# Optimization experiments

Hardware: AMD Instinct MI355X
Metric: run time of the kernel (lower is better)

## Reference

```python
import jax, jax.numpy as jnp
import numpy as np

N = 50000   # nodes
E = 800000  # edges
F = 128     # num_features
H = 128     # n_hidden_channels
C = 16      # num_classes


def _gcn_conv(x, W, b, src, dst, dinv):
    """PyG GCNConv: h = x @ W; out = D^-1/2 (A+I) D^-1/2 h + b."""
    h = x @ W                                   # [N, out]
    coef = dinv[src] * dinv[dst]                # [E]
    msg = h[src] * coef[:, None]                # gather + scale
    agg = jax.ops.segment_sum(msg, dst, num_segments=N)
    agg = agg + h * (dinv * dinv)[:, None]      # self-loop term
    return agg + b


def setup_inputs() -> dict:
    key = jax.random.key(0)
    ks = jax.random.split(key, 8)
    x = jax.random.normal(ks[0], (N, F), dtype=jnp.float32)
    edge_index = jax.random.randint(ks[1], (2, E), 0, N, dtype=jnp.int64)

    def glorot(k, fan_in, fan_out):
        return jax.random.normal(k, (fan_in, fan_out), dtype=jnp.float32) / np.sqrt(fan_in)

    return {
        "x": x,
        "edge_index": edge_index,
        "W1": glorot(ks[2], F, H), "b1": jnp.zeros((H,), jnp.float32),
        "W2": glorot(ks[3], H, H), "b2": jnp.zeros((H,), jnp.float32),
        "W3": glorot(ks[4], H, H), "b3": jnp.zeros((H,), jnp.float32),
        "W4": glorot(ks[5], H, C), "b4": jnp.zeros((C,), jnp.float32),
        "Wc": glorot(ks[6], C, 1), "bc": jnp.zeros((1,), jnp.float32),
    }


def reference(x, edge_index, W1, b1, W2, b2, W3, b3, W4, b4, Wc, bc):
    src, dst = edge_index[0], edge_index[1]
    # degree with self-loops (edge_weight = 1)
    deg = jax.ops.segment_sum(jnp.ones((E,), x.dtype), dst, num_segments=N) + 1.0
    dinv = jax.lax.rsqrt(deg)

    out = _gcn_conv(x, W1, b1, src, dst, dinv)
    out = jnp.tanh(_gcn_conv(out, W2, b2, src, dst, dinv))
    out = jax.nn.leaky_relu(_gcn_conv(out, W3, b3, src, dst, dinv), negative_slope=0.01)
    out = jax.nn.leaky_relu(_gcn_conv(out, W4, b4, src, dst, dinv), negative_slope=0.01)
    out = jax.nn.elu(out @ Wc + bc)             # [N, 1]
    return out
```

## Files before the change

### kernel.cpp

```cpp
#include <hip/hip_runtime.h>
#include <hip/hip_bf16.h>
#include <cstdint>
#include <cstddef>

#define NN 50000
#define NE 800000

using short8v = __attribute__((ext_vector_type(8))) short;
using f32x4 = __attribute__((ext_vector_type(4))) float;

__device__ __forceinline__ unsigned short f2bf(float f) {
    unsigned u = __float_as_uint(f);
    u += 0x7fffu + ((u >> 16) & 1u);
    return (unsigned short)(u >> 16);
}
__device__ __forceinline__ float bf2f(unsigned s) {
    return __uint_as_float(s << 16);
}


__global__ __launch_bounds__(256) void zero_i32(int* __restrict__ p, int n) {
    int i = blockIdx.x * 256 + threadIdx.x;
    if (i < n) p[i] = 0;
}

__global__ __launch_bounds__(256) void count_deg_rank(const int* __restrict__ dst,
                                                      int* __restrict__ cntP,
                                                      int* __restrict__ rank, int E) {
    int e = blockIdx.x * 256 + threadIdx.x;
    if (e < E) {
        int d = dst[e];
        rank[e] = atomicAdd(&cntP[d << 4], 1);
    }
}

__global__ __launch_bounds__(1024) void scan1(const int* __restrict__ cntP,
                                              int* __restrict__ local,
                                              int* __restrict__ bsum,
                                              float* __restrict__ dinv, int N) {
    int t = threadIdx.x;
    int g = blockIdx.x * 1024 + t;
    int lane = t & 63, w = t >> 6;
    int v = (g < N) ? cntP[g << 4] : 0;
    if (g < N) dinv[g] = rsqrtf((float)v + 1.0f);
    int x = v;
    #pragma unroll
    for (int off = 1; off < 64; off <<= 1) {
        int y = __shfl_up(x, off);
        if (lane >= off) x += y;
    }
    __shared__ int wsum[16];
    if (lane == 63) wsum[w] = x;
    __syncthreads();
    if (t < 16) {
        int s = wsum[t];
        int xx = s;
        #pragma unroll
        for (int off = 1; off < 16; off <<= 1) {
            int y = __shfl_up(xx, off);
            if (t >= off) xx += y;
        }
        wsum[t] = xx - s;
    }
    __syncthreads();
    int excl = wsum[w] + x - v;
    if (g < N) local[g] = excl;
    if (t == 1023) bsum[blockIdx.x] = excl + v;
}

__global__ __launch_bounds__(64) void scan2(int* __restrict__ bsum, int NB) {
    int t = threadIdx.x;
    int v = (t < NB) ? bsum[t] : 0;
    int x = v;
    #pragma unroll
    for (int off = 1; off < 64; off <<= 1) {
        int y = __shfl_up(x, off);
        if (t >= off) x += y;
    }
    if (t < NB) bsum[t] = x - v;
}

__global__ __launch_bounds__(256) void scan3(const int* __restrict__ local,
                                             const int* __restrict__ bsum,
                                             int* __restrict__ rowptr, int N, int E) {
    int g = blockIdx.x * 256 + threadIdx.x;
    if (g < N) rowptr[g] = local[g] + bsum[g >> 10];
    if (g == 0) rowptr[N] = E;
}

__global__ __launch_bounds__(256) void scatter_plain(const int* __restrict__ src,
                                                     const int* __restrict__ dst,
                                                     const int* __restrict__ rowptr,
                                                     const int* __restrict__ rank,
                                                     int* __restrict__ csr, int E) {
    int e = blockIdx.x * 256 + threadIdx.x;
    if (e < E) {
        int d = dst[e];
        csr[rowptr[d] + rank[e]] = src[e];
    }
}


__global__ __launch_bounds__(256) void split_wt(const float* __restrict__ Wa,
                                                const float* __restrict__ Wb,
                                                const float* __restrict__ Wc,
                                                unsigned short* __restrict__ WTh,
                                                unsigned short* __restrict__ WTl) {
    const float* W = (blockIdx.y == 0) ? Wa : (blockIdx.y == 1) ? Wb : Wc;
    int i = blockIdx.x * 256 + threadIdx.x;
    int n = i >> 7, k = i & 127;
    float v = W[k * 128 + n];
    unsigned short h = f2bf(v);
    float lo = v - bf2f(h);
    size_t base = (size_t)blockIdx.y * 16384 + i;
    WTh[base] = h;
    WTl[base] = f2bf(lo);
}


template <bool F32IN>
__global__ __launch_bounds__(256) void gemm_mfma(const void* __restrict__ Xin,
                                                 const void* __restrict__ Xlin,
                                                 const unsigned short* __restrict__ WTh,
                                                 const unsigned short* __restrict__ WTl,
                                                 const float* __restrict__ dinv,
                                                 float* __restrict__ out, int N) {
    __shared__ unsigned short xh[64 * 128];
    __shared__ unsigned short xl[64 * 128];
    int tid = threadIdx.x;
    int lane = tid & 63, wv = tid >> 6;
    int row0 = blockIdx.x * 64;

    #pragma unroll
    for (int i = 0; i < 4; ++i) {
        int id = i * 256 + tid;
        int r = id >> 4, kc = id & 15;
        uint4 vh = make_uint4(0, 0, 0, 0), vl = make_uint4(0, 0, 0, 0);
        if (row0 + r < N) {
            if constexpr (F32IN) {
                const float* Xf = (const float*)Xin;
                float4 a = *(const float4*)(Xf + (size_t)(row0 + r) * 128 + kc * 8);
                float4 b = *(const float4*)(Xf + (size_t)(row0 + r) * 128 + kc * 8 + 4);
                unsigned short h0 = f2bf(a.x), h1 = f2bf(a.y), h2 = f2bf(a.z), h3 = f2bf(a.w);
                unsigned short h4 = f2bf(b.x), h5 = f2bf(b.y), h6 = f2bf(b.z), h7 = f2bf(b.w);
                vh = make_uint4((unsigned)h0 | ((unsigned)h1 << 16),
                                (unsigned)h2 | ((unsigned)h3 << 16),
                                (unsigned)h4 | ((unsigned)h5 << 16),
                                (unsigned)h6 | ((unsigned)h7 << 16));
                vl = make_uint4((unsigned)f2bf(a.x - bf2f(h0)) | ((unsigned)f2bf(a.y - bf2f(h1)) << 16),
                                (unsigned)f2bf(a.z - bf2f(h2)) | ((unsigned)f2bf(a.w - bf2f(h3)) << 16),
                                (unsigned)f2bf(b.x - bf2f(h4)) | ((unsigned)f2bf(b.y - bf2f(h5)) << 16),
                                (unsigned)f2bf(b.z - bf2f(h6)) | ((unsigned)f2bf(b.w - bf2f(h7)) << 16));
            } else {
                vh = *(const uint4*)&((const unsigned*)Xin)[(size_t)(row0 + r) * 64 + kc * 4];
                vl = *(const uint4*)&((const unsigned*)Xlin)[(size_t)(row0 + r) * 64 + kc * 4];
            }
        }
        int off = r * 128 + ((kc * 8) ^ ((r & 7) << 3));
        *(uint4*)&xh[off] = vh;
        *(uint4*)&xl[off] = vl;
    }
    __syncthreads();

    int mstrip = (wv & 1) * 32;
    int nbase = (wv >> 1) * 64;
    f32x4 acc[2][4] = {};

    #pragma unroll
    for (int ks = 0; ks < 4; ++ks) {
        short8v afh[2], afl[2];
        #pragma unroll
        for (int mt = 0; mt < 2; ++mt) {
            int r = mstrip + mt * 16 + (lane & 15);
            int off = r * 128 + ((ks * 32 + ((lane >> 4) * 8)) ^ ((r & 7) << 3));
            afh[mt] = *(const short8v*)&xh[off];
            afl[mt] = *(const short8v*)&xl[off];
        }
        #pragma unroll
        for (int nt = 0; nt < 4; ++nt) {
            int c = nbase + nt * 16 + (lane & 15);
            size_t goff = (size_t)c * 128 + ks * 32 + (lane >> 4) * 8;
            short8v bfh = *(const short8v*)&WTh[goff];
            short8v bfl = *(const short8v*)&WTl[goff];
            #pragma unroll
            for (int mt = 0; mt < 2; ++mt) {
                acc[mt][nt] = __builtin_amdgcn_mfma_f32_16x16x32_bf16(afh[mt], bfh, acc[mt][nt], 0, 0, 0);
                acc[mt][nt] = __builtin_amdgcn_mfma_f32_16x16x32_bf16(afh[mt], bfl, acc[mt][nt], 0, 0, 0);
                acc[mt][nt] = __builtin_amdgcn_mfma_f32_16x16x32_bf16(afl[mt], bfh, acc[mt][nt], 0, 0, 0);
            }
        }
    }

    #pragma unroll
    for (int mt = 0; mt < 2; ++mt) {
        #pragma unroll
        for (int i = 0; i < 4; ++i) {
            int r = row0 + mstrip + mt * 16 + (lane >> 4) * 4 + i;
            if (r < N) {
                float dv = dinv[r];
                #pragma unroll
                for (int nt = 0; nt < 4; ++nt) {
                    int cg = nbase + nt * 16 + (lane & 15);
                    out[(size_t)r * 128 + cg] = acc[mt][nt][i] * dv;
                }
            }
        }
    }
}

__global__ __launch_bounds__(256) void gemm16(const unsigned* __restrict__ Xh,
                                              const unsigned* __restrict__ Xl,
                                              const float* __restrict__ W,
                                              const float* __restrict__ dinv,
                                              float* __restrict__ out, int N) {
    __shared__ float xs[64][128];
    __shared__ float ws4[128][16];
    int tid = threadIdx.x;
    int row0 = blockIdx.x * 64;

    #pragma unroll
    for (int i = 0; i < 2; ++i)
        ((float4*)ws4)[i * 256 + tid] = ((const float4*)W)[i * 256 + tid];

    #pragma unroll
    for (int i = 0; i < 8; ++i) {
        int id = i * 256 + tid;
        int r = id >> 5, c4 = id & 31;
        float4 v = make_float4(0.f, 0.f, 0.f, 0.f);
        if (row0 + r < N) {
            uint2 hh = *(const uint2*)&Xh[(size_t)(row0 + r) * 64 + c4 * 2];
            uint2 ll = *(const uint2*)&Xl[(size_t)(row0 + r) * 64 + c4 * 2];
            v.x = bf2f(hh.x & 0xffffu) + bf2f(ll.x & 0xffffu);
            v.y = bf2f(hh.x >> 16) + bf2f(ll.x >> 16);
            v.z = bf2f(hh.y & 0xffffu) + bf2f(ll.y & 0xffffu);
            v.w = bf2f(hh.y >> 16) + bf2f(ll.y >> 16);
        }
        *(float4*)&xs[r][c4 * 4] = v;
    }
    __syncthreads();

    int ty = tid >> 4, tx = tid & 15;
    float acc[4] = {};
    #pragma unroll 4
    for (int k = 0; k < 128; ++k) {
        float wvv = ws4[k][tx];
        #pragma unroll
        for (int i = 0; i < 4; ++i)
            acc[i] = fmaf(xs[ty * 4 + i][k], wvv, acc[i]);
    }
    #pragma unroll
    for (int i = 0; i < 4; ++i) {
        int r = row0 + ty * 4 + i;
        if (r < N) out[(size_t)r * 16 + tx] = acc[i] * dinv[r];
    }
}


template <int ACT>
__global__ __launch_bounds__(256) void agg128(const float* __restrict__ HS,
                                              const int* __restrict__ rp,
                                              const int* __restrict__ csr,
                                              const float* __restrict__ dinv,
                                              const float* __restrict__ b,
                                              unsigned* __restrict__ Xh,
                                              unsigned* __restrict__ Xl, int N) {
    int wid = threadIdx.x >> 6, lane = threadIdx.x & 63;
    int n = blockIdx.x * 4 + wid;
    if (n >= N) return;
    const float2* H2 = (const float2*)HS;
    float2 a0 = H2[(size_t)n * 64 + lane];
    float2 a1 = make_float2(0.f, 0.f), a2 = a1, a3 = a1;
    float2 a4 = a1, a5 = a1, a6 = a1, a7 = a1;
    int e = rp[n], end = rp[n + 1];
    for (; e + 8 <= end; e += 8) {
        int s0 = csr[e], s1 = csr[e + 1], s2 = csr[e + 2], s3 = csr[e + 3];
        int s4 = csr[e + 4], s5 = csr[e + 5], s6 = csr[e + 6], s7 = csr[e + 7];
        float2 v0 = H2[(size_t)s0 * 64 + lane];
        float2 v1 = H2[(size_t)s1 * 64 + lane];
        float2 v2 = H2[(size_t)s2 * 64 + lane];
        float2 v3 = H2[(size_t)s3 * 64 + lane];
        float2 v4 = H2[(size_t)s4 * 64 + lane];
        float2 v5 = H2[(size_t)s5 * 64 + lane];
        float2 v6 = H2[(size_t)s6 * 64 + lane];
        float2 v7 = H2[(size_t)s7 * 64 + lane];
        a0.x += v0.x; a0.y += v0.y; a1.x += v1.x; a1.y += v1.y;
        a2.x += v2.x; a2.y += v2.y; a3.x += v3.x; a3.y += v3.y;
        a4.x += v4.x; a4.y += v4.y; a5.x += v5.x; a5.y += v5.y;
        a6.x += v6.x; a6.y += v6.y; a7.x += v7.x; a7.y += v7.y;
    }
    if (e + 4 <= end) {
        int s0 = csr[e], s1 = csr[e + 1], s2 = csr[e + 2], s3 = csr[e + 3];
        float2 v0 = H2[(size_t)s0 * 64 + lane];
        float2 v1 = H2[(size_t)s1 * 64 + lane];
        float2 v2 = H2[(size_t)s2 * 64 + lane];
        float2 v3 = H2[(size_t)s3 * 64 + lane];
        a4.x += v0.x; a4.y += v0.y; a5.x += v1.x; a5.y += v1.y;
        a6.x += v2.x; a6.y += v2.y; a7.x += v3.x; a7.y += v3.y;
        e += 4;
    }
    for (; e < end; ++e) {
        int s = csr[e];
        float2 v = H2[(size_t)s * 64 + lane];
        a0.x += v.x; a0.y += v.y;
    }
    float accx = ((a0.x + a1.x) + (a2.x + a3.x)) + ((a4.x + a5.x) + (a6.x + a7.x));
    float accy = ((a0.y + a1.y) + (a2.y + a3.y)) + ((a4.y + a5.y) + (a6.y + a7.y));
    float dv = dinv[n];
    float2 bb = ((const float2*)b)[lane];
    float ox = fmaf(dv, accx, bb.x);
    float oy = fmaf(dv, accy, bb.y);
    if (ACT == 1) { ox = tanhf(ox); oy = tanhf(oy); }
    else if (ACT == 2) {
        ox = ox > 0.f ? ox : 0.01f * ox;
        oy = oy > 0.f ? oy : 0.01f * oy;
    }
    unsigned short h0 = f2bf(ox), h1 = f2bf(oy);
    float l0 = ox - bf2f(h0), l1 = oy - bf2f(h1);
    Xh[(size_t)n * 64 + lane] = (unsigned)h0 | ((unsigned)h1 << 16);
    Xl[(size_t)n * 64 + lane] = (unsigned)f2bf(l0) | ((unsigned)f2bf(l1) << 16);
}


__global__ __launch_bounds__(256) void final_layer(const float* __restrict__ HS4,
                                                   const int* __restrict__ rp,
                                                   const int* __restrict__ csr,
                                                   const float* __restrict__ dinv,
                                                   const float* __restrict__ b4,
                                                   const float* __restrict__ Wc,
                                                   const float* __restrict__ bc,
                                                   float* __restrict__ out, int N) {
    int wid = threadIdx.x >> 6, lane = threadIdx.x & 63;
    int n = blockIdx.x * 4 + wid;
    if (n >= N) return;
    int f = lane & 15, g = lane >> 4;
    float acc = 0.f;
    int beg = rp[n], end = rp[n + 1];
    for (int e = beg + g; e < end; e += 4)
        acc += HS4[(size_t)csr[e] * 16 + f];
    acc += __shfl_xor(acc, 16);
    acc += __shfl_xor(acc, 32);
    acc += HS4[(size_t)n * 16 + f];
    float t = fmaf(dinv[n], acc, b4[f]);
    t = t > 0.f ? t : 0.01f * t;
    float p = t * Wc[f];
    p += __shfl_xor(p, 1);
    p += __shfl_xor(p, 2);
    p += __shfl_xor(p, 4);
    p += __shfl_xor(p, 8);
    if (lane == 0) {
        float z = p + bc[0];
        out[n] = z > 0.f ? z : expm1f(z);
    }
}


extern "C" void kernel_launch(void* const* d_in, const int* in_sizes, int n_in,
                              void* d_out, int out_size, void* d_ws, size_t ws_size,
                              hipStream_t stream) {
    const int N = NN, E = NE;
    const float* x  = (const float*)d_in[0];
    const int*   ei = (const int*)d_in[1];
    const float* W1 = (const float*)d_in[2];
    const float* b1 = (const float*)d_in[3];
    const float* W2 = (const float*)d_in[4];
    const float* b2 = (const float*)d_in[5];
    const float* W3 = (const float*)d_in[6];
    const float* b3 = (const float*)d_in[7];
    const float* W4 = (const float*)d_in[8];
    const float* b4 = (const float*)d_in[9];
    const float* Wc = (const float*)d_in[10];
    const float* bc = (const float*)d_in[11];
    float* out = (float*)d_out;
    const int* src = ei;
    const int* dst = ei + E;

    char* p = (char*)d_ws;
    auto carve = [&](size_t bytes) -> char* {
        char* q = p;
        p += (bytes + 255) & ~(size_t)255;
        return q;
    };
    int*            cntP   = (int*)carve((size_t)N * 16 * 4);
    int*            rank   = (int*)carve((size_t)E * 4);
    int*            rowptr = (int*)carve((size_t)(N + 1) * 4);
    float*          dinv   = (float*)carve((size_t)N * 4);
    int*            csr    = (int*)carve((size_t)E * 4);
    int*            locsc  = (int*)carve((size_t)N * 4);
    int*            bsum   = (int*)carve((size_t)64 * 4);
    unsigned short* WTh    = (unsigned short*)carve((size_t)3 * 16384 * 2);
    unsigned short* WTl    = (unsigned short*)carve((size_t)3 * 16384 * 2);
    unsigned*       Xh     = (unsigned*)carve((size_t)N * 64 * 4);
    unsigned*       Xl     = (unsigned*)carve((size_t)N * 64 * 4);
    float*          bufB   = (float*)carve((size_t)N * 128 * 4);

    const int NB = (N + 1023) / 1024;

    zero_i32<<<(N * 16 + 255) / 256, 256, 0, stream>>>(cntP, N * 16);
    count_deg_rank<<<(E + 255) / 256, 256, 0, stream>>>(dst, cntP, rank, E);
    scan1<<<NB, 1024, 0, stream>>>(cntP, locsc, bsum, dinv, N);
    scan2<<<1, 64, 0, stream>>>(bsum, NB);
    scan3<<<(N + 255) / 256, 256, 0, stream>>>(locsc, bsum, rowptr, N, E);
    scatter_plain<<<(E + 255) / 256, 256, 0, stream>>>(src, dst, rowptr, rank, csr, E);
    split_wt<<<dim3(64, 3), 256, 0, stream>>>(W1, W2, W3, WTh, WTl);

    int gblocks = (N + 63) / 64;
    int ablocks = (N + 3) / 4;

    gemm_mfma<true><<<gblocks, 256, 0, stream>>>(x, nullptr, WTh, WTl, dinv, bufB, N);
    agg128<0><<<ablocks, 256, 0, stream>>>(bufB, rowptr, csr, dinv, b1, Xh, Xl, N);
    gemm_mfma<false><<<gblocks, 256, 0, stream>>>(Xh, Xl, WTh + 16384, WTl + 16384, dinv, bufB, N);
    agg128<1><<<ablocks, 256, 0, stream>>>(bufB, rowptr, csr, dinv, b2, Xh, Xl, N);
    gemm_mfma<false><<<gblocks, 256, 0, stream>>>(Xh, Xl, WTh + 32768, WTl + 32768, dinv, bufB, N);
    agg128<2><<<ablocks, 256, 0, stream>>>(bufB, rowptr, csr, dinv, b3, Xh, Xl, N);
    gemm16<<<gblocks, 256, 0, stream>>>(Xh, Xl, W4, dinv, bufB, N);
    final_layer<<<ablocks, 256, 0, stream>>>(bufB, rowptr, csr, dinv, b4, Wc, bc, out, N);
}
```

Before: 348.7 us.

## Merge setup kernels and stage weight tiles through LDS in GEMM

Replaces the zero kernel with hipMemsetAsync, folds the single-block scan2 into each scan3 block, and merges the weight-split kernel into the CSR scatter kernel as extra blocks. Together these cut several kernel launches from the preprocessing chain. The MFMA GEMM now loads each 32-wide K slice of the transposed weights into padded shared memory, instead of reading B fragments directly from global memory. That adds two barriers per K step and extra LDS use, which may lower occupancy.

New measurement: 330.8 us. -5.1%, faster.

```diff
diff --git a/kernel.cpp b/kernel.cpp
--- a/kernel.cpp
+++ b/kernel.cpp
@@ -18,11 +18,6 @@
     return __uint_as_float(s << 16);
 }
 
-
-__global__ __launch_bounds__(256) void zero_i32(int* __restrict__ p, int n) {
-    int i = blockIdx.x * 256 + threadIdx.x;
-    if (i < n) p[i] = 0;
-}
 
 __global__ __launch_bounds__(256) void count_deg_rank(const int* __restrict__ dst,
                                                       int* __restrict__ cntP,
@@ -68,53 +63,56 @@
     if (t == 1023) bsum[blockIdx.x] = excl + v;
 }
 
-__global__ __launch_bounds__(64) void scan2(int* __restrict__ bsum, int NB) {
-    int t = threadIdx.x;
-    int v = (t < NB) ? bsum[t] : 0;
-    int x = v;
-    #pragma unroll
-    for (int off = 1; off < 64; off <<= 1) {
-        int y = __shfl_up(x, off);
-        if (t >= off) x += y;
-    }
-    if (t < NB) bsum[t] = x - v;
-}
-
 __global__ __launch_bounds__(256) void scan3(const int* __restrict__ local,
                                              const int* __restrict__ bsum,
-                                             int* __restrict__ rowptr, int N, int E) {
-    int g = blockIdx.x * 256 + threadIdx.x;
-    if (g < N) rowptr[g] = local[g] + bsum[g >> 10];
+                                             int* __restrict__ rowptr,
+                                             int N, int E, int NB) {
+    __shared__ int sb[64];
+    int t = threadIdx.x;
+    if (t < 64) {
+        int v = (t < NB) ? bsum[t] : 0;
+        int x = v;
+        #pragma unroll
+        for (int off = 1; off < 64; off <<= 1) {
+            int y = __shfl_up(x, off);
+            if (t >= off) x += y;
+        }
+        sb[t] = x - v;
+    }
+    __syncthreads();
+    int g = blockIdx.x * 256 + t;
+    if (g < N) rowptr[g] = local[g] + sb[g >> 10];
     if (g == 0) rowptr[N] = E;
 }
 
-__global__ __launch_bounds__(256) void scatter_plain(const int* __restrict__ src,
+__global__ __launch_bounds__(256) void scatter_split(const int* __restrict__ src,
                                                      const int* __restrict__ dst,
                                                      const int* __restrict__ rowptr,
                                                      const int* __restrict__ rank,
-                                                     int* __restrict__ csr, int E) {
-    int e = blockIdx.x * 256 + threadIdx.x;
-    if (e < E) {
-        int d = dst[e];
-        csr[rowptr[d] + rank[e]] = src[e];
-    }
-}
-
-
-__global__ __launch_bounds__(256) void split_wt(const float* __restrict__ Wa,
-                                                const float* __restrict__ Wb,
-                                                const float* __restrict__ Wc,
-                                                unsigned short* __restrict__ WTh,
-                                                unsigned short* __restrict__ WTl) {
-    const float* W = (blockIdx.y == 0) ? Wa : (blockIdx.y == 1) ? Wb : Wc;
-    int i = blockIdx.x * 256 + threadIdx.x;
-    int n = i >> 7, k = i & 127;
-    float v = W[k * 128 + n];
-    unsigned short h = f2bf(v);
-    float lo = v - bf2f(h);
-    size_t base = (size_t)blockIdx.y * 16384 + i;
-    WTh[base] = h;
-    WTl[base] = f2bf(lo);
+                                                     int* __restrict__ csr, int E,
+                                                     int sblocks,
+                                                     const float* __restrict__ Wa,
+                                                     const float* __restrict__ Wb,
+                                                     const float* __restrict__ Wc,
+                                                     unsigned short* __restrict__ WTh,
+                                                     unsigned short* __restrict__ WTl) {
+    if ((int)blockIdx.x < sblocks) {
+        int e = blockIdx.x * 256 + threadIdx.x;
+        if (e < E) {
+            int d = dst[e];
+            csr[rowptr[d] + rank[e]] = src[e];
+        }
+    } else {
+        int i = (blockIdx.x - sblocks) * 256 + threadIdx.x;
+        int j = i >> 14;
+        int idx = i & 16383;
+        int n = idx >> 7, k = idx & 127;
+        const float* W = (j == 0) ? Wa : (j == 1) ? Wb : Wc;
+        float v = W[k * 128 + n];
+        unsigned short h = f2bf(v);
+        WTh[i] = h;
+        WTl[i] = f2bf(v - bf2f(h));
+    }
 }
 
 
@@ -127,6 +125,8 @@
                                                  float* __restrict__ out, int N) {
     __shared__ unsigned short xh[64 * 128];
     __shared__ unsigned short xl[64 * 128];
+    __shared__ unsigned short wh[128 * 40];
+    __shared__ unsigned short wl[128 * 40];
     int tid = threadIdx.x;
     int lane = tid & 63, wv = tid >> 6;
     int row0 = blockIdx.x * 64;
@@ -160,14 +160,24 @@
         *(uint4*)&xh[off] = vh;
         *(uint4*)&xl[off] = vl;
     }
-    __syncthreads();
 
     int mstrip = (wv & 1) * 32;
     int nbase = (wv >> 1) * 64;
     f32x4 acc[2][4] = {};
 
-    #pragma unroll
     for (int ks = 0; ks < 4; ++ks) {
+        __syncthreads();
+        #pragma unroll
+        for (int i = 0; i < 2; ++i) {
+            int id = i * 256 + tid;
+            int n = id >> 2, q = id & 3;
+            *(uint4*)&wh[n * 40 + q * 8] =
+                *(const uint4*)&WTh[(size_t)n * 128 + ks * 32 + q * 8];
+            *(uint4*)&wl[n * 40 + q * 8] =
+                *(const uint4*)&WTl[(size_t)n * 128 + ks * 32 + q * 8];
+        }
+        __syncthreads();
+
         short8v afh[2], afl[2];
         #pragma unroll
         for (int mt = 0; mt < 2; ++mt) {
@@ -179,9 +189,9 @@
         #pragma unroll
         for (int nt = 0; nt < 4; ++nt) {
             int c = nbase + nt * 16 + (lane & 15);
-            size_t goff = (size_t)c * 128 + ks * 32 + (lane >> 4) * 8;
-            short8v bfh = *(const short8v*)&WTh[goff];
-            short8v bfl = *(const short8v*)&WTl[goff];
+            int boff = c * 40 + (lane >> 4) * 8;
+            short8v bfh = *(const short8v*)&wh[boff];
+            short8v bfl = *(const short8v*)&wl[boff];
             #pragma unroll
             for (int mt = 0; mt < 2; ++mt) {
                 acc[mt][nt] = __builtin_amdgcn_mfma_f32_16x16x32_bf16(afh[mt], bfh, acc[mt][nt], 0, 0, 0);
@@ -394,14 +404,15 @@
     float*          bufB   = (float*)carve((size_t)N * 128 * 4);
 
     const int NB = (N + 1023) / 1024;
-
-    zero_i32<<<(N * 16 + 255) / 256, 256, 0, stream>>>(cntP, N * 16);
-    count_deg_rank<<<(E + 255) / 256, 256, 0, stream>>>(dst, cntP, rank, E);
+    const int sblocks = (E + 255) / 256;
+    const int wblocks = (3 * 16384) / 256;
+
+    hipMemsetAsync(cntP, 0, (size_t)N * 16 * 4, stream);
+    count_deg_rank<<<sblocks, 256, 0, stream>>>(dst, cntP, rank, E);
     scan1<<<NB, 1024, 0, stream>>>(cntP, locsc, bsum, dinv, N);
-    scan2<<<1, 64, 0, stream>>>(bsum, NB);
-    scan3<<<(N + 255) / 256, 256, 0, stream>>>(locsc, bsum, rowptr, N, E);
-    scatter_plain<<<(E + 255) / 256, 256, 0, stream>>>(src, dst, rowptr, rank, csr, E);
-    split_wt<<<dim3(64, 3), 256, 0, stream>>>(W1, W2, W3, WTh, WTl);
+    scan3<<<(N + 255) / 256, 256, 0, stream>>>(locsc, bsum, rowptr, N, E, NB);
+    scatter_split<<<sblocks + wblocks, 256, 0, stream>>>(src, dst, rowptr, rank, csr, E,
+                                                         sblocks, W1, W2, W3, WTh, WTl);
 
     int gblocks = (N + 63) / 64;
     int ablocks = (N + 3) / 4;
```
